# Performance work log

Measured on AMD Instinct MI355X. Metric: run time of the kernel, lower is better.

The kernel has to match this reference:

```python
import jax, jax.numpy as jnp
import numpy as np

D_MODEL = 512
HEADS = 8
WIN = 16
LN_EPS = 1e-5


def setup_inputs() -> dict:
    key = jax.random.key(0)
    ks = jax.random.split(key, 5)
    B, T = 2, 4096
    s = 1.0 / np.sqrt(D_MODEL)
    x = jax.random.normal(ks[0], (B, T, D_MODEL), dtype=jnp.float32)
    Wq = jax.random.normal(ks[1], (D_MODEL, D_MODEL), dtype=jnp.float32) * s
    Wk = jax.random.normal(ks[2], (D_MODEL, D_MODEL), dtype=jnp.float32) * s
    Wv = jax.random.normal(ks[3], (D_MODEL, D_MODEL), dtype=jnp.float32) * s
    Wp = jax.random.normal(ks[4], (D_MODEL, D_MODEL), dtype=jnp.float32) * s
    ln_gamma = jnp.ones((D_MODEL,), dtype=jnp.float32)
    ln_beta = jnp.zeros((D_MODEL,), dtype=jnp.float32)
    return {"x": x, "Wq": Wq, "Wk": Wk, "Wv": Wv, "Wp": Wp,
            "ln_gamma": ln_gamma, "ln_beta": ln_beta}


def _local_attention(x, Wq, Wk, Wv, Wp, ln_gamma, ln_beta):
    B, T, D = x.shape
    H = HEADS
    d = D // H
    scale = d ** (-0.5)
    # projections (torch Linear: y = x @ W^T)
    q = (x @ Wq.T).reshape(B, T, H, d)
    k = (x @ Wk.T).reshape(B, T, H, d)
    v = (x @ Wv.T).reshape(B, T, H, d)
    offs = jnp.arange(-WIN, WIN + 1)                      # [W]
    pos = jnp.arange(T)[:, None] + offs[None, :]          # [T, W]
    valid = (pos >= 0) & (pos < T)                        # [T, W]
    idx = jnp.clip(pos, 0, T - 1)                         # [T, W]
    k_win = k[:, idx]                                     # [B, T, W, H, d]
    v_win = v[:, idx]                                     # [B, T, W, H, d]
    scores = jnp.einsum('bthd,btwhd->bthw', q, k_win) * scale
    scores = jnp.where(valid[None, :, None, :], scores, -jnp.inf)
    attn = jax.nn.softmax(scores, axis=-1)                # over window
    out = jnp.einsum('bthw,btwhd->bthd', attn, v_win).reshape(B, T, D)
    y = x + out @ Wp.T                                    # residual + proj
    mu = jnp.mean(y, axis=-1, keepdims=True)
    var = jnp.mean(jnp.square(y - mu), axis=-1, keepdims=True)
    return ln_gamma * (y - mu) * jax.lax.rsqrt(var + LN_EPS) + ln_beta


def reference(x, Wq, Wk, Wv, Wp, ln_gamma, ln_beta):
    return _local_attention(x, Wq, Wk, Wv, Wp, ln_gamma, ln_beta)
```

## Files before the change

### kernel.cpp

```cpp
#include <hip/hip_runtime.h>
#include <hip/hip_bf16.h>
#include <stdint.h>

typedef __bf16 bf16;
typedef __attribute__((ext_vector_type(8))) __bf16 bf16x8;
typedef __attribute__((ext_vector_type(2))) __bf16 bf16x2;
typedef __attribute__((ext_vector_type(4))) float f32x4;
typedef __attribute__((ext_vector_type(4))) unsigned int u32x4;

#define GLOAD16(gsrc, ldst)                                              \
  __builtin_amdgcn_global_load_lds(                                      \
      (const __attribute__((address_space(1))) unsigned int*)(gsrc),     \
      (__attribute__((address_space(3))) unsigned int*)(ldst), 16, 0, 0)

static constexpr int T_LEN = 4096;
static constexpr int WIN = 16;

__device__ __forceinline__ bf16x8 cvt8(float4 a, float4 b) {
  bf16x8 o;
  o[0] = (bf16)a.x; o[1] = (bf16)a.y; o[2] = (bf16)a.z; o[3] = (bf16)a.w;
  o[4] = (bf16)b.x; o[5] = (bf16)b.y; o[6] = (bf16)b.z; o[7] = (bf16)b.w;
  return o;
}

__global__ __launch_bounds__(256) void prep_kernel(const float* __restrict__ x,
                                                   const float* __restrict__ wq,
                                                   const float* __restrict__ wk,
                                                   const float* __restrict__ wv,
                                                   const float* __restrict__ wp,
                                                   bf16* __restrict__ xb,
                                                   bf16* __restrict__ wqkv,
                                                   bf16* __restrict__ wpb) {
  int bid = blockIdx.x;
  if (bid < 2048) {
    int i = bid * 256 + threadIdx.x;
    const float4* s4 = (const float4*)x + (size_t)i * 2;
    ((bf16x8*)xb)[i] = cvt8(s4[0], s4[1]);
  } else {
    int i = (bid - 2048) * 256 + threadIdx.x;
    int which = i >> 15;
    int j = i & 32767;
    const float* src = (which == 0) ? wq : (which == 1) ? wk : (which == 2) ? wv : wp;
    bf16* dst = (which < 3) ? (wqkv + (size_t)which * 512 * 512) : wpb;
    const float4* s4 = (const float4*)src + (size_t)j * 2;
    ((bf16x8*)dst)[j] = cvt8(s4[0], s4[1]);
  }
}

__global__ __launch_bounds__(256) void gemm_qkv_kernel(const bf16* __restrict__ Ab,
                                                       const bf16* __restrict__ Bw,
                                                       bf16* __restrict__ Cb) {
  constexpr int K = 512, BK = 64, NIT = K / BK;
  __shared__ __align__(16) bf16 As[8192];
  __shared__ __align__(16) bf16 Bs[4096];
  const int tid = threadIdx.x;
  const int l = tid & 63;
  const int w = tid >> 6;
  const int g = l >> 4;
  const int c = l & 15;
  int bid = blockIdx.x;
  bid = (bid & 7) * 192 + (bid >> 3);
  const int m0 = (bid / 24) * 128;
  const int n0 = (bid % 24) * 64;

  const int wm = (w >> 1) * 64;
  const int wn = (w & 1) * 32;
  const int cx = c & 7;

  const f32x4 zero = {0.f, 0.f, 0.f, 0.f};
  f32x4 acc[4][2];
#pragma unroll
  for (int i = 0; i < 4; ++i)
#pragma unroll
    for (int j = 0; j < 2; ++j) acc[i][j] = zero;

#pragma unroll 1
  for (int t = 0; t < NIT; ++t) {
    const int k0 = t * BK;
#pragma unroll
    for (int i = 0; i < 4; ++i) {
      int s = tid + i * 256;
      int row = s >> 3;
      int j = s & 7;
      GLOAD16(Ab + (size_t)(m0 + row) * 512 + k0 + ((j ^ (row & 7)) << 3),
              &As[s * 8]);
    }
#pragma unroll
    for (int i = 0; i < 2; ++i) {
      int s = tid + i * 256;
      int row = s >> 3;
      int j = s & 7;
      GLOAD16(Bw + (size_t)(n0 + row) * 512 + k0 + ((j ^ (row & 7)) << 3),
              &Bs[s * 8]);
    }
    __syncthreads();
#pragma unroll
    for (int kk = 0; kk < 2; ++kk) {
      const int joff = ((kk * 4 + g) ^ cx) << 3;
      bf16x8 af[4], bfr[2];
#pragma unroll
      for (int mi = 0; mi < 4; ++mi)
        af[mi] = *(const bf16x8*)&As[(wm + mi * 16 + c) * 64 + joff];
#pragma unroll
      for (int ni = 0; ni < 2; ++ni)
        bfr[ni] = *(const bf16x8*)&Bs[(wn + ni * 16 + c) * 64 + joff];
#pragma unroll
      for (int mi = 0; mi < 4; ++mi)
#pragma unroll
        for (int ni = 0; ni < 2; ++ni)
          acc[mi][ni] = __builtin_amdgcn_mfma_f32_16x16x32_bf16(af[mi], bfr[ni], acc[mi][ni], 0, 0, 0);
    }
    __syncthreads();
  }

  bf16* Cw = &As[w * 2048];
  const int r0 = (l >> 4) * 4;
#pragma unroll
  for (int mi = 0; mi < 4; ++mi)
#pragma unroll
    for (int ni = 0; ni < 2; ++ni)
#pragma unroll
      for (int r = 0; r < 4; ++r)
        Cw[(mi * 16 + r0 + r) * 32 + ni * 16 + c] = (bf16)acc[mi][ni][r];
#pragma unroll
  for (int i = 0; i < 4; ++i) {
    int row = (l >> 2) + 16 * i;
    bf16x8 v = *(const bf16x8*)&Cw[row * 32 + (l & 3) * 8];
    *(bf16x8*)(Cb + (size_t)(m0 + wm + row) * 1536 + n0 + wn + (l & 3) * 8) = v;
  }
}

__global__ __launch_bounds__(512) void attn_proj_ln_kernel(
    const bf16* __restrict__ qkv, const bf16* __restrict__ Bw,
    const float* __restrict__ X, const float* __restrict__ gamma,
    const float* __restrict__ beta, float* __restrict__ out) {
  __shared__ __align__(16) bf16 POOL[63744];
  bf16* KV = POOL;
  bf16* Pp = POOL + 36864;
  bf16* aoutL = POOL + 46080;
  float* rsum = (float*)(POOL + 62720);
  float* rsq  = (float*)(POOL + 63232);

  const int tid = threadIdx.x;
  const int w = tid >> 6;
  const int l = tid & 63;
  const int g = l >> 4;
  const int c = l & 15;
  const int cx = c & 7;
  int bid = blockIdx.x;
  bid = (bid & 7) * 32 + (bid >> 3);
  const int m0 = bid * 32;
  const int b = m0 >> 12;
  const int tloc0 = m0 & (T_LEN - 1);
  const int base = b * T_LEN;

  const f32x4 zero = {0.f, 0.f, 0.f, 0.f};
  const u32x4 zu = {0u, 0u, 0u, 0u};
  const float scale = 0.125f;

  if (tid < 256) {
    int hl = tid >> 6;
    int row = tid & 63;
    *(uint4*)&KV[18432 + hl * 4608 + row * 72 + 64] = make_uint4(0u, 0u, 0u, 0u);
  }

#pragma unroll 1
  for (int pass = 0; pass < 2; ++pass) {
    if (pass) __syncthreads();
#pragma unroll
    for (int i = 0; i < 4; ++i) {
      int task = tid + i * 512;
      int hl = task >> 9;
      int rem = task & 511;
      int pp = rem >> 3;
      int c8 = (rem & 7) * 8;
      int h = pass * 4 + hl;
      int pg = base + min(max(tloc0 - WIN + pp, 0), T_LEN - 1);
      const bf16* kr = qkv + (size_t)pg * 1536 + 512 + h * 64 + c8;
      const bf16* vr = qkv + (size_t)pg * 1536 + 1024 + h * 64 + c8;
      *(bf16x8*)&KV[hl * 4608 + pp * 72 + c8] = *(const bf16x8*)kr;
      bf16x8 vv = *(const bf16x8*)vr;
      bf16* vt = &KV[18432 + hl * 4608];
#pragma unroll
      for (int e = 0; e < 8; ++e) vt[(c8 + e) * 72 + pp] = vv[e];
    }
    __syncthreads();

    const int hl = w >> 1;
    const int wh = w & 1;
    const int h = pass * 4 + hl;
    const int tg = tloc0 + wh * 16;
    bf16* Kl = &KV[hl * 4608];
    bf16* Vt = &KV[18432 + hl * 4608];

    const bf16* qrow = qkv + (size_t)(base + tg + c) * 1536 + h * 64;
    bf16x8 qf0 = *(const bf16x8*)(qrow + g * 8);
    bf16x8 qf1 = *(const bf16x8*)(qrow + 32 + g * 8);

    f32x4 st[3];
#pragma unroll
    for (int wt = 0; wt < 3; ++wt) {
      int rk = 16 * wh + 16 * wt + c;
      bf16x8 ka0 = *(const bf16x8*)&Kl[rk * 72 + g * 8];
      bf16x8 ka1 = *(const bf16x8*)&Kl[rk * 72 + 32 + g * 8];
      f32x4 t = __builtin_amdgcn_mfma_f32_16x16x32_bf16(ka0, qf0, zero, 0, 0, 0);
      st[wt] = __builtin_amdgcn_mfma_f32_16x16x32_bf16(ka1, qf1, t, 0, 0, 0);
    }

    float pv[3][4];
    float lsum = 0.f;
#pragma unroll
    for (int wt = 0; wt < 3; ++wt)
#pragma unroll
      for (int r = 0; r < 4; ++r) {
        int ww = 16 * wt + 4 * g + r;
        int pos = tg - WIN + ww;
        bool valid = (ww >= c) && (ww <= c + 32) && (pos >= 0) && (pos < T_LEN);
        float e = __expf(st[wt][r] * scale);
        pv[wt][r] = valid ? e : 0.f;
        lsum += pv[wt][r];
      }
    lsum += __shfl_xor(lsum, 16);
    lsum += __shfl_xor(lsum, 32);
    float inv = 1.f / lsum;

    bf16* P = &Pp[w * 1152];
#pragma unroll
    for (int wt = 0; wt < 3; ++wt) {
      bf16x2 p01, p23;
      p01[0] = (bf16)(pv[wt][0] * inv);
      p01[1] = (bf16)(pv[wt][1] * inv);
      p23[0] = (bf16)(pv[wt][2] * inv);
      p23[1] = (bf16)(pv[wt][3] * inv);
      *(bf16x2*)&P[c * 56 + 16 * wt + 4 * g]     = p01;
      *(bf16x2*)&P[c * 56 + 16 * wt + 4 * g + 2] = p23;
    }

    bf16x8 pa0 = *(const bf16x8*)&P[c * 56 + 8 * g];
    int g1 = (g < 2) ? g : 1;
    bf16x8 pa1 = *(const bf16x8*)&P[c * 56 + 32 + 8 * g1];
    if (g >= 2) pa1 = __builtin_bit_cast(bf16x8, zu);

    const int off0 = 16 * wh + 8 * g;
    const int off1 = 16 * wh + ((g < 2) ? 32 + 8 * g : 48);
    f32x4 acc[4] = {zero, zero, zero, zero};
#pragma unroll
    for (int dt = 0; dt < 4; ++dt) {
      bf16x8 v0 = *(const bf16x8*)&Vt[(16 * dt + c) * 72 + off0];
      bf16x8 v1 = *(const bf16x8*)&Vt[(16 * dt + c) * 72 + off1];
      acc[dt] = __builtin_amdgcn_mfma_f32_16x16x32_bf16(pa0, v0, acc[dt], 0, 0, 0);
      acc[dt] = __builtin_amdgcn_mfma_f32_16x16x32_bf16(pa1, v1, acc[dt], 0, 0, 0);
    }

#pragma unroll
    for (int dt = 0; dt < 4; ++dt)
#pragma unroll
      for (int r = 0; r < 4; ++r)
        aoutL[(wh * 16 + 4 * g + r) * 520 + h * 64 + 16 * dt + c] = (bf16)acc[dt][r];
  }
  __syncthreads();

  f32x4 acc2[2][4];
#pragma unroll
  for (int m = 0; m < 2; ++m)
#pragma unroll
    for (int n = 0; n < 4; ++n) acc2[m][n] = zero;

#pragma unroll 1
  for (int t = 0; t < 8; ++t) {
    const int k0 = t * 64;
#pragma unroll
    for (int i = 0; i < 8; ++i) {
      int s = tid + i * 512;
      int row = s >> 3;
      int j = s & 7;
      GLOAD16(Bw + (size_t)row * 512 + k0 + ((j ^ (row & 7)) << 3), &KV[s * 8]);
    }
    __syncthreads();
#pragma unroll
    for (int kk = 0; kk < 2; ++kk) {
      const int joff = ((kk * 4 + g) ^ cx) << 3;
      bf16x8 af[2], bfv[4];
#pragma unroll
      for (int m = 0; m < 2; ++m)
        af[m] = *(const bf16x8*)&aoutL[(m * 16 + c) * 520 + k0 + (kk * 4 + g) * 8];
#pragma unroll
      for (int n = 0; n < 4; ++n)
        bfv[n] = *(const bf16x8*)&KV[(w * 64 + n * 16 + c) * 64 + joff];
#pragma unroll
      for (int m = 0; m < 2; ++m)
#pragma unroll
        for (int n = 0; n < 4; ++n)
          acc2[m][n] = __builtin_amdgcn_mfma_f32_16x16x32_bf16(af[m], bfv[n], acc2[m][n], 0, 0, 0);
    }
    __syncthreads();
  }

  const int col0 = w * 64 + c;
  float ps[2][4], ps2[2][4];
#pragma unroll
  for (int m = 0; m < 2; ++m)
#pragma unroll
    for (int r = 0; r < 4; ++r) {
      int row = m0 + m * 16 + 4 * g + r;
      float s = 0.f, s2 = 0.f;
#pragma unroll
      for (int n = 0; n < 4; ++n) {
        float y = acc2[m][n][r] + X[(size_t)row * 512 + col0 + n * 16];
        acc2[m][n][r] = y;
        s += y;
        s2 += y * y;
      }
      ps[m][r] = s;
      ps2[m][r] = s2;
    }
#pragma unroll
  for (int m = 0; m < 2; ++m)
#pragma unroll
    for (int r = 0; r < 4; ++r) {
      float s = ps[m][r], s2 = ps2[m][r];
      s += __shfl_xor(s, 1);  s2 += __shfl_xor(s2, 1);
      s += __shfl_xor(s, 2);  s2 += __shfl_xor(s2, 2);
      s += __shfl_xor(s, 4);  s2 += __shfl_xor(s2, 4);
      s += __shfl_xor(s, 8);  s2 += __shfl_xor(s2, 8);
      ps[m][r] = s;
      ps2[m][r] = s2;
    }
  if (c == 0) {
#pragma unroll
    for (int m = 0; m < 2; ++m)
#pragma unroll
      for (int r = 0; r < 4; ++r) {
        rsum[(m * 16 + 4 * g + r) * 8 + w] = ps[m][r];
        rsq[(m * 16 + 4 * g + r) * 8 + w] = ps2[m][r];
      }
  }
  __syncthreads();

  float gam[4], bet[4];
#pragma unroll
  for (int n = 0; n < 4; ++n) {
    gam[n] = gamma[col0 + n * 16];
    bet[n] = beta[col0 + n * 16];
  }
#pragma unroll
  for (int m = 0; m < 2; ++m)
#pragma unroll
    for (int r = 0; r < 4; ++r) {
      int rl = m * 16 + 4 * g + r;
      float sum = 0.f, sq = 0.f;
#pragma unroll
      for (int j = 0; j < 8; ++j) {
        sum += rsum[rl * 8 + j];
        sq += rsq[rl * 8 + j];
      }
      float mu = sum * (1.f / 512.f);
      float var = sq * (1.f / 512.f) - mu * mu;
      float rs = rsqrtf(var + 1e-5f);
#pragma unroll
      for (int n = 0; n < 4; ++n)
        out[(size_t)(m0 + rl) * 512 + col0 + n * 16] =
            gam[n] * (acc2[m][n][r] - mu) * rs + bet[n];
    }
}

extern "C" void kernel_launch(void* const* d_in, const int* in_sizes, int n_in,
                              void* d_out, int out_size, void* d_ws, size_t ws_size,
                              hipStream_t stream) {
  const float* x  = (const float*)d_in[0];
  const float* Wq = (const float*)d_in[1];
  const float* Wk = (const float*)d_in[2];
  const float* Wv = (const float*)d_in[3];
  const float* Wp = (const float*)d_in[4];
  const float* g  = (const float*)d_in[5];
  const float* be = (const float*)d_in[6];
  float* out = (float*)d_out;

  char* ws = (char*)d_ws;
  bf16* xb   = (bf16*)(ws);
  bf16* wqkv = (bf16*)(ws + 8388608);
  bf16* wpb  = (bf16*)(ws + 9961472);
  bf16* qkv  = (bf16*)(ws + 10485760);

  prep_kernel<<<2560, 256, 0, stream>>>(x, Wq, Wk, Wv, Wp, xb, wqkv, wpb);
  gemm_qkv_kernel<<<1536, 256, 0, stream>>>(xb, wqkv, qkv);
  attn_proj_ln_kernel<<<256, 512, 0, stream>>>(qkv, wpb, x, g, be, out);
}
```

Baseline: 55.29 us.

## Halve attention tile to 16 rows, 256 threads, read Wp directly from global

Restructures the fused attention+projection+LayerNorm kernel so each block handles 16 query rows with 4 waves (one head per wave per pass) instead of 32 rows with 8 waves. This doubles the grid to 512 blocks and shrinks LDS to raise occupancy. The projection GEMM now streams Wp fragments straight from global memory rather than staging them through LDS with barriers. The V transpose store is rotated per lane to reduce LDS bank conflicts. The trade-off is more total global/L2 traffic for Wp, which is now re-read by every block without LDS reuse, and higher register use with eight accumulators per wave.

```diff
diff --git a/kernel.cpp b/kernel.cpp
--- a/kernel.cpp
+++ b/kernel.cpp
@@ -130,26 +130,25 @@
   }
 }
 
-__global__ __launch_bounds__(512) void attn_proj_ln_kernel(
+__global__ __launch_bounds__(256) void attn_proj_ln_kernel(
     const bf16* __restrict__ qkv, const bf16* __restrict__ Bw,
     const float* __restrict__ X, const float* __restrict__ gamma,
     const float* __restrict__ beta, float* __restrict__ out) {
-  __shared__ __align__(16) bf16 POOL[63744];
+  __shared__ __align__(16) bf16 POOL[40320];
   bf16* KV = POOL;
-  bf16* Pp = POOL + 36864;
-  bf16* aoutL = POOL + 46080;
-  float* rsum = (float*)(POOL + 62720);
-  float* rsq  = (float*)(POOL + 63232);
+  bf16* Pp = POOL + 28160;
+  bf16* aoutL = POOL + 31744;
+  float* rsum = (float*)(POOL + 40064);
+  float* rsq  = (float*)(POOL + 40192);
 
   const int tid = threadIdx.x;
   const int w = tid >> 6;
   const int l = tid & 63;
   const int g = l >> 4;
   const int c = l & 15;
-  const int cx = c & 7;
   int bid = blockIdx.x;
-  bid = (bid & 7) * 32 + (bid >> 3);
-  const int m0 = bid * 32;
+  bid = (bid & 7) * 64 + (bid >> 3);
+  const int m0 = bid * 16;
   const int b = m0 >> 12;
   const int tloc0 = m0 & (T_LEN - 1);
   const int base = b * T_LEN;
@@ -158,49 +157,50 @@
   const u32x4 zu = {0u, 0u, 0u, 0u};
   const float scale = 0.125f;
 
-  if (tid < 256) {
+  {
     int hl = tid >> 6;
     int row = tid & 63;
-    *(uint4*)&KV[18432 + hl * 4608 + row * 72 + 64] = make_uint4(0u, 0u, 0u, 0u);
+    *(uint4*)&KV[hl * 7040 + 3456 + row * 56 + 48] = make_uint4(0u, 0u, 0u, 0u);
   }
 
 #pragma unroll 1
   for (int pass = 0; pass < 2; ++pass) {
     if (pass) __syncthreads();
 #pragma unroll
-    for (int i = 0; i < 4; ++i) {
-      int task = tid + i * 512;
-      int hl = task >> 9;
-      int rem = task & 511;
+    for (int i = 0; i < 6; ++i) {
+      int task = tid + i * 256;
+      int hl = task / 384;
+      int rem = task - hl * 384;
       int pp = rem >> 3;
       int c8 = (rem & 7) * 8;
       int h = pass * 4 + hl;
       int pg = base + min(max(tloc0 - WIN + pp, 0), T_LEN - 1);
       const bf16* kr = qkv + (size_t)pg * 1536 + 512 + h * 64 + c8;
       const bf16* vr = qkv + (size_t)pg * 1536 + 1024 + h * 64 + c8;
-      *(bf16x8*)&KV[hl * 4608 + pp * 72 + c8] = *(const bf16x8*)kr;
+      *(bf16x8*)&KV[hl * 7040 + pp * 72 + c8] = *(const bf16x8*)kr;
       bf16x8 vv = *(const bf16x8*)vr;
-      bf16* vt = &KV[18432 + hl * 4608];
-#pragma unroll
-      for (int e = 0; e < 8; ++e) vt[(c8 + e) * 72 + pp] = vv[e];
+      bf16* vt = &KV[hl * 7040 + 3456];
+      int rot = (c8 >> 3) & 7;
+#pragma unroll
+      for (int e = 0; e < 8; ++e) {
+        int er = (e + rot) & 7;
+        vt[(c8 + er) * 56 + pp] = vv[er];
+      }
     }
     __syncthreads();
 
-    const int hl = w >> 1;
-    const int wh = w & 1;
-    const int h = pass * 4 + hl;
-    const int tg = tloc0 + wh * 16;
-    bf16* Kl = &KV[hl * 4608];
-    bf16* Vt = &KV[18432 + hl * 4608];
-
-    const bf16* qrow = qkv + (size_t)(base + tg + c) * 1536 + h * 64;
+    const int h = pass * 4 + w;
+    bf16* Kl = &KV[w * 7040];
+    bf16* Vt = &KV[w * 7040 + 3456];
+
+    const bf16* qrow = qkv + (size_t)(base + tloc0 + c) * 1536 + h * 64;
     bf16x8 qf0 = *(const bf16x8*)(qrow + g * 8);
     bf16x8 qf1 = *(const bf16x8*)(qrow + 32 + g * 8);
 
     f32x4 st[3];
 #pragma unroll
     for (int wt = 0; wt < 3; ++wt) {
-      int rk = 16 * wh + 16 * wt + c;
+      int rk = 16 * wt + c;
       bf16x8 ka0 = *(const bf16x8*)&Kl[rk * 72 + g * 8];
       bf16x8 ka1 = *(const bf16x8*)&Kl[rk * 72 + 32 + g * 8];
       f32x4 t = __builtin_amdgcn_mfma_f32_16x16x32_bf16(ka0, qf0, zero, 0, 0, 0);
@@ -214,7 +214,7 @@
 #pragma unroll
       for (int r = 0; r < 4; ++r) {
         int ww = 16 * wt + 4 * g + r;
-        int pos = tg - WIN + ww;
+        int pos = tloc0 - WIN + ww;
         bool valid = (ww >= c) && (ww <= c + 32) && (pos >= 0) && (pos < T_LEN);
         float e = __expf(st[wt][r] * scale);
         pv[wt][r] = valid ? e : 0.f;
@@ -224,7 +224,7 @@
     lsum += __shfl_xor(lsum, 32);
     float inv = 1.f / lsum;
 
-    bf16* P = &Pp[w * 1152];
+    bf16* P = &Pp[w * 896];
 #pragma unroll
     for (int wt = 0; wt < 3; ++wt) {
       bf16x2 p01, p23;
@@ -241,13 +241,13 @@
     bf16x8 pa1 = *(const bf16x8*)&P[c * 56 + 32 + 8 * g1];
     if (g >= 2) pa1 = __builtin_bit_cast(bf16x8, zu);
 
-    const int off0 = 16 * wh + 8 * g;
-    const int off1 = 16 * wh + ((g < 2) ? 32 + 8 * g : 48);
+    const int off0 = 8 * g;
+    const int off1 = (g < 2) ? 32 + 8 * g : 48;
     f32x4 acc[4] = {zero, zero, zero, zero};
 #pragma unroll
     for (int dt = 0; dt < 4; ++dt) {
-      bf16x8 v0 = *(const bf16x8*)&Vt[(16 * dt + c) * 72 + off0];
-      bf16x8 v1 = *(const bf16x8*)&Vt[(16 * dt + c) * 72 + off1];
+      bf16x8 v0 = *(const bf16x8*)&Vt[(16 * dt + c) * 56 + off0];
+      bf16x8 v1 = *(const bf16x8*)&Vt[(16 * dt + c) * 56 + off1];
       acc[dt] = __builtin_amdgcn_mfma_f32_16x16x32_bf16(pa0, v0, acc[dt], 0, 0, 0);
       acc[dt] = __builtin_amdgcn_mfma_f32_16x16x32_bf16(pa1, v1, acc[dt], 0, 0, 0);
     }
@@ -256,112 +256,77 @@
     for (int dt = 0; dt < 4; ++dt)
 #pragma unroll
       for (int r = 0; r < 4; ++r)
-        aoutL[(wh * 16 + 4 * g + r) * 520 + h * 64 + 16 * dt + c] = (bf16)acc[dt][r];
+        aoutL[(4 * g + r) * 520 + h * 64 + 16 * dt + c] = (bf16)acc[dt][r];
   }
   __syncthreads();
 
-  f32x4 acc2[2][4];
-#pragma unroll
-  for (int m = 0; m < 2; ++m)
-#pragma unroll
-    for (int n = 0; n < 4; ++n) acc2[m][n] = zero;
-
-#pragma unroll 1
-  for (int t = 0; t < 8; ++t) {
-    const int k0 = t * 64;
-#pragma unroll
-    for (int i = 0; i < 8; ++i) {
-      int s = tid + i * 512;
-      int row = s >> 3;
-      int j = s & 7;
-      GLOAD16(Bw + (size_t)row * 512 + k0 + ((j ^ (row & 7)) << 3), &KV[s * 8]);
-    }
-    __syncthreads();
-#pragma unroll
-    for (int kk = 0; kk < 2; ++kk) {
-      const int joff = ((kk * 4 + g) ^ cx) << 3;
-      bf16x8 af[2], bfv[4];
-#pragma unroll
-      for (int m = 0; m < 2; ++m)
-        af[m] = *(const bf16x8*)&aoutL[(m * 16 + c) * 520 + k0 + (kk * 4 + g) * 8];
-#pragma unroll
-      for (int n = 0; n < 4; ++n)
-        bfv[n] = *(const bf16x8*)&KV[(w * 64 + n * 16 + c) * 64 + joff];
-#pragma unroll
-      for (int m = 0; m < 2; ++m)
-#pragma unroll
-        for (int n = 0; n < 4; ++n)
-          acc2[m][n] = __builtin_amdgcn_mfma_f32_16x16x32_bf16(af[m], bfv[n], acc2[m][n], 0, 0, 0);
-    }
-    __syncthreads();
-  }
-
-  const int col0 = w * 64 + c;
-  float ps[2][4], ps2[2][4];
-#pragma unroll
-  for (int m = 0; m < 2; ++m)
+  const int wcol = w * 128;
+  f32x4 acc2[8];
+#pragma unroll
+  for (int n = 0; n < 8; ++n) acc2[n] = zero;
+
+#pragma unroll
+  for (int kt = 0; kt < 16; ++kt) {
+    bf16x8 af = *(const bf16x8*)&aoutL[c * 520 + kt * 32 + g * 8];
+#pragma unroll
+    for (int n = 0; n < 8; ++n) {
+      bf16x8 bfv = *(const bf16x8*)(Bw + (size_t)(wcol + n * 16 + c) * 512 +
+                                    kt * 32 + g * 8);
+      acc2[n] = __builtin_amdgcn_mfma_f32_16x16x32_bf16(af, bfv, acc2[n], 0, 0, 0);
+    }
+  }
+
+  float ps[4], ps2[4];
+#pragma unroll
+  for (int r = 0; r < 4; ++r) {
+    int row = m0 + 4 * g + r;
+    float s = 0.f, s2 = 0.f;
+#pragma unroll
+    for (int n = 0; n < 8; ++n) {
+      float y = acc2[n][r] + X[(size_t)row * 512 + wcol + n * 16 + c];
+      acc2[n][r] = y;
+      s += y;
+      s2 += y * y;
+    }
+    ps[r] = s;
+    ps2[r] = s2;
+  }
+#pragma unroll
+  for (int r = 0; r < 4; ++r) {
+    float s = ps[r], s2 = ps2[r];
+    s += __shfl_xor(s, 1);  s2 += __shfl_xor(s2, 1);
+    s += __shfl_xor(s, 2);  s2 += __shfl_xor(s2, 2);
+    s += __shfl_xor(s, 4);  s2 += __shfl_xor(s2, 4);
+    s += __shfl_xor(s, 8);  s2 += __shfl_xor(s2, 8);
+    ps[r] = s;
+    ps2[r] = s2;
+  }
+  if (c == 0) {
 #pragma unroll
     for (int r = 0; r < 4; ++r) {
-      int row = m0 + m * 16 + 4 * g + r;
-      float s = 0.f, s2 = 0.f;
-#pragma unroll
-      for (int n = 0; n < 4; ++n) {
-        float y = acc2[m][n][r] + X[(size_t)row * 512 + col0 + n * 16];
-        acc2[m][n][r] = y;
-        s += y;
-        s2 += y * y;
-      }
-      ps[m][r] = s;
-      ps2[m][r] = s2;
-    }
-#pragma unroll
-  for (int m = 0; m < 2; ++m)
-#pragma unroll
-    for (int r = 0; r < 4; ++r) {
-      float s = ps[m][r], s2 = ps2[m][r];
-      s += __shfl_xor(s, 1);  s2 += __shfl_xor(s2, 1);
-      s += __shfl_xor(s, 2);  s2 += __shfl_xor(s2, 2);
-      s += __shfl_xor(s, 4);  s2 += __shfl_xor(s2, 4);
-      s += __shfl_xor(s, 8);  s2 += __shfl_xor(s2, 8);
-      ps[m][r] = s;
-      ps2[m][r] = s2;
-    }
-  if (c == 0) {
-#pragma unroll
-    for (int m = 0; m < 2; ++m)
-#pragma unroll
-      for (int r = 0; r < 4; ++r) {
-        rsum[(m * 16 + 4 * g + r) * 8 + w] = ps[m][r];
-        rsq[(m * 16 + 4 * g + r) * 8 + w] = ps2[m][r];
-      }
+      rsum[(4 * g + r) * 4 + w] = ps[r];
+      rsq[(4 * g + r) * 4 + w] = ps2[r];
+    }
   }
   __syncthreads();
 
-  float gam[4], bet[4];
-#pragma unroll
-  for (int n = 0; n < 4; ++n) {
-    gam[n] = gamma[col0 + n * 16];
-    bet[n] = beta[col0 + n * 16];
-  }
-#pragma unroll
-  for (int m = 0; m < 2; ++m)
-#pragma unroll
-    for (int r = 0; r < 4; ++r) {
-      int rl = m * 16 + 4 * g + r;
-      float sum = 0.f, sq = 0.f;
-#pragma unroll
-      for (int j = 0; j < 8; ++j) {
-        sum += rsum[rl * 8 + j];
-        sq += rsq[rl * 8 + j];
-      }
-      float mu = sum * (1.f / 512.f);
-      float var = sq * (1.f / 512.f) - mu * mu;
-      float rs = rsqrtf(var + 1e-5f);
-#pragma unroll
-      for (int n = 0; n < 4; ++n)
-        out[(size_t)(m0 + rl) * 512 + col0 + n * 16] =
-            gam[n] * (acc2[m][n][r] - mu) * rs + bet[n];
-    }
+#pragma unroll
+  for (int r = 0; r < 4; ++r) {
+    int rl = 4 * g + r;
+    float4 sv = *(const float4*)&rsum[rl * 4];
+    float4 qv = *(const float4*)&rsq[rl * 4];
+    float sum = (sv.x + sv.y) + (sv.z + sv.w);
+    float sq  = (qv.x + qv.y) + (qv.z + qv.w);
+    float mu = sum * (1.f / 512.f);
+    float var = sq * (1.f / 512.f) - mu * mu;
+    float rs = rsqrtf(var + 1e-5f);
+#pragma unroll
+    for (int n = 0; n < 8; ++n) {
+      int col = wcol + n * 16 + c;
+      out[(size_t)(m0 + rl) * 512 + col] =
+          gamma[col] * (acc2[n][r] - mu) * rs + beta[col];
+    }
+  }
 }
 
 extern "C" void kernel_launch(void* const* d_in, const int* in_sizes, int n_in,
@@ -384,5 +349,5 @@
 
   prep_kernel<<<2560, 256, 0, stream>>>(x, Wq, Wk, Wv, Wp, xb, wqkv, wpb);
   gemm_qkv_kernel<<<1536, 256, 0, stream>>>(xb, wqkv, qkv);
-  attn_proj_ln_kernel<<<256, 512, 0, stream>>>(qkv, wpb, x, g, be, out);
-}
+  attn_proj_ln_kernel<<<512, 256, 0, stream>>>(qkv, wpb, x, g, be, out);
+}
```

Measured after the change: 70.98 us. 28.4% more time.

## Prepack Wp into chunk-major layout and load projection B directly from global

Applied to the files above, without the earlier changes.

The prep kernel now writes the bf16 Wp weight in a chunk-major layout, with 8-element k-chunks contiguous across output rows. The attention+proj kernel then reads its B fragments straight from global/L2 as coalesced 16-byte loads instead of staging them through LDS with global_load_lds and barriers. The projection k-loop is fully unrolled and loses its two __syncthreads per iteration. In exchange, every block re-reads Wp from cache without LDS reuse across waves, and global load latency is exposed to the MFMA chain.

```diff
diff --git a/kernel.cpp b/kernel.cpp
--- a/kernel.cpp
+++ b/kernel.cpp
@@ -40,10 +40,17 @@
     int i = (bid - 2048) * 256 + threadIdx.x;
     int which = i >> 15;
     int j = i & 32767;
-    const float* src = (which == 0) ? wq : (which == 1) ? wk : (which == 2) ? wv : wp;
-    bf16* dst = (which < 3) ? (wqkv + (size_t)which * 512 * 512) : wpb;
-    const float4* s4 = (const float4*)src + (size_t)j * 2;
-    ((bf16x8*)dst)[j] = cvt8(s4[0], s4[1]);
+    if (which < 3) {
+      const float* src = (which == 0) ? wq : (which == 1) ? wk : wv;
+      bf16* dst = wqkv + (size_t)which * 512 * 512;
+      const float4* s4 = (const float4*)src + (size_t)j * 2;
+      ((bf16x8*)dst)[j] = cvt8(s4[0], s4[1]);
+    } else {
+      int chunk = j >> 9;
+      int row = j & 511;
+      const float4* s4 = (const float4*)(wp + (size_t)row * 512 + chunk * 8);
+      ((bf16x8*)wpb)[j] = cvt8(s4[0], s4[1]);
+    }
   }
 }
 
@@ -131,7 +138,7 @@
 }
 
 __global__ __launch_bounds__(512) void attn_proj_ln_kernel(
-    const bf16* __restrict__ qkv, const bf16* __restrict__ Bw,
+    const bf16* __restrict__ qkv, const bf16* __restrict__ Bp,
     const float* __restrict__ X, const float* __restrict__ gamma,
     const float* __restrict__ beta, float* __restrict__ out) {
   __shared__ __align__(16) bf16 POOL[63744];
@@ -146,7 +153,6 @@
   const int l = tid & 63;
   const int g = l >> 4;
   const int c = l & 15;
-  const int cx = c & 7;
   int bid = blockIdx.x;
   bid = (bid & 7) * 32 + (bid >> 3);
   const int m0 = bid * 32;
@@ -182,7 +188,8 @@
       bf16x8 vv = *(const bf16x8*)vr;
       bf16* vt = &KV[18432 + hl * 4608];
 #pragma unroll
-      for (int e = 0; e < 8; ++e) vt[(c8 + e) * 72 + pp] = vv[e];
+      for (int e = 0; e < 8; ++e)
+        vt[(c8 + e) * 72 + pp] = vv[e];
     }
     __syncthreads();
 
@@ -266,34 +273,24 @@
 #pragma unroll
     for (int n = 0; n < 4; ++n) acc2[m][n] = zero;
 
-#pragma unroll 1
+#pragma unroll
   for (int t = 0; t < 8; ++t) {
-    const int k0 = t * 64;
-#pragma unroll
-    for (int i = 0; i < 8; ++i) {
-      int s = tid + i * 512;
-      int row = s >> 3;
-      int j = s & 7;
-      GLOAD16(Bw + (size_t)row * 512 + k0 + ((j ^ (row & 7)) << 3), &KV[s * 8]);
-    }
-    __syncthreads();
 #pragma unroll
     for (int kk = 0; kk < 2; ++kk) {
-      const int joff = ((kk * 4 + g) ^ cx) << 3;
+      const int chunk = t * 8 + kk * 4 + g;
       bf16x8 af[2], bfv[4];
 #pragma unroll
       for (int m = 0; m < 2; ++m)
-        af[m] = *(const bf16x8*)&aoutL[(m * 16 + c) * 520 + k0 + (kk * 4 + g) * 8];
+        af[m] = *(const bf16x8*)&aoutL[(m * 16 + c) * 520 + chunk * 8];
 #pragma unroll
       for (int n = 0; n < 4; ++n)
-        bfv[n] = *(const bf16x8*)&KV[(w * 64 + n * 16 + c) * 64 + joff];
+        bfv[n] = *(const bf16x8*)(Bp + ((size_t)chunk * 512 + w * 64 + n * 16 + c) * 8);
 #pragma unroll
       for (int m = 0; m < 2; ++m)
 #pragma unroll
         for (int n = 0; n < 4; ++n)
           acc2[m][n] = __builtin_amdgcn_mfma_f32_16x16x32_bf16(af[m], bfv[n], acc2[m][n], 0, 0, 0);
     }
-    __syncthreads();
   }
 
   const int col0 = w * 64 + c;
```

Measured after the change: 50.77 us (median of 3 runs). -8.2%, faster.
